# Optimization experiments

Measured on AMD Instinct MI355X. Metric: run time of the kernel, lower is better.

Reference implementation:

```python
import jax, jax.numpy as jnp
import numpy as np

EPS = 1e-5


def conv_bn_relu(x, W, b, g, be):
    # 3x3 SAME conv, NCHW / OIHW, followed by training-mode BatchNorm and ReLU
    y = jax.lax.conv_general_dilated(
        x, W, window_strides=(1, 1), padding='SAME',
        dimension_numbers=('NCHW', 'OIHW', 'NCHW'))
    y = y + b[None, :, None, None]
    m = y.mean(axis=(0, 2, 3), keepdims=True)
    v = y.var(axis=(0, 2, 3), keepdims=True)  # biased var, as torch BN uses
    y = (y - m) * jax.lax.rsqrt(v + EPS)
    y = y * g[None, :, None, None] + be[None, :, None, None]
    return jax.nn.relu(y)


def setup_inputs() -> dict:
    key = jax.random.key(0)
    ks = jax.random.split(key, 16)
    B, M, D = 512, 256, 100
    inp = {
        'F_channel': jax.random.normal(ks[0], (B, 2, 20, 20), jnp.float32),
        'G_real': jax.random.normal(ks[1], (B, M, D), jnp.float32),
        'G_imag': jax.random.normal(ks[2], (B, M, D), jnp.float32),
        'hr_real': jax.random.normal(ks[3], (B, D), jnp.float32),
        'hr_imag': jax.random.normal(ks[4], (B, D), jnp.float32),
    }
    chans = [(2, 128), (128, 64), (64, 64), (64, 32)]
    for i, (ci, co) in enumerate(chans):
        fan = ci * 9
        inp[f'W{i+1}'] = jax.random.normal(ks[5 + i], (co, ci, 3, 3), jnp.float32) / np.sqrt(fan)
        inp[f'b{i+1}'] = jnp.zeros((co,), jnp.float32)
        inp[f'g{i+1}'] = jnp.ones((co,), jnp.float32)
        inp[f'be{i+1}'] = jnp.zeros((co,), jnp.float32)
    inp['Wo'] = jax.random.normal(ks[9], (200, 12800), jnp.float32) / np.sqrt(12800)
    inp['bo'] = jnp.zeros((200,), jnp.float32)
    return inp


def reference(F_channel, G_real, G_imag, hr_real, hr_imag,
              W1, b1, g1, be1, W2, b2, g2, be2,
              W3, b3, g3, be3, W4, b4, g4, be4, Wo, bo):
    out = conv_bn_relu(F_channel, W1, b1, g1, be1)
    out = conv_bn_relu(out, W2, b2, g2, be2)
    out = conv_bn_relu(out, W3, b3, g3, be3)
    out = conv_bn_relu(out, W4, b4, g4, be4)
    out = out.reshape(out.shape[0], -1)          # [B, 12800], NCHW flatten matches torch view
    out = out @ Wo.T + bo                        # [B, 200]

    theta1, theta2 = out[:, :100], out[:, 100:]
    c = jnp.cos(theta1)                          # Re(Theta)  [B, D]
    s = jnp.sin(theta2)                          # Im(Theta)  [B, D]

    # diag_embed + matmul == elementwise scale of G columns by Theta (complex)
    Ar = G_real * c[:, None, :] - G_imag * s[:, None, :]   # [B, M, D]
    Ai = G_real * s[:, None, :] + G_imag * c[:, None, :]

    # matmul with hr (complex): t2 = sum_d A[b,m,d] * hr[b,d]
    t2r = jnp.einsum('bmd,bd->bm', Ar, hr_real) - jnp.einsum('bmd,bd->bm', Ai, hr_imag)
    t2i = jnp.einsum('bmd,bd->bm', Ar, hr_imag) + jnp.einsum('bmd,bd->bm', Ai, hr_real)

    B = out.shape[0]  # D_row = Theta.size(0) = batch
    norm_sq = jnp.sum(t2r * t2r + t2i * t2i)
    return -norm_sq / B
```

## Files before the change

kernel.cpp:

```cpp
#include <hip/hip_runtime.h>
#include <math.h>

typedef __bf16 bf16x8 __attribute__((ext_vector_type(8)));
typedef float f32x4 __attribute__((ext_vector_type(4)));
typedef unsigned short ushort8 __attribute__((ext_vector_type(8)));

__device__ __forceinline__ float bf2f(unsigned short u){ return __uint_as_float(((unsigned)u) << 16); }
__device__ __forceinline__ unsigned short f2bf(float f){
  unsigned v = __float_as_uint(f);
  return (unsigned short)((v + 0x7FFFu + ((v >> 16) & 1u)) >> 16);
}

__global__ void packw1_kernel(const float* __restrict__ W1, unsigned short* __restrict__ Wpk1)
{
  int idx = blockIdx.x*256 + threadIdx.x;
  if (idx >= 512) return;
  int lane = idx & 63, ct = idx >> 6;
  int co = ct*16 + (lane & 15);
  int lq = lane >> 4;
#pragma unroll
  for (int j = 0; j < 8; ++j){
    int k = lq*8 + j;
    Wpk1[(size_t)idx*8 + j] = (k < 18) ? f2bf(W1[(size_t)co*18 + k]) : (unsigned short)0;
  }
}

__global__ __launch_bounds__(256, 2) void conv1_mfma(
    const float* __restrict__ F, const unsigned short* __restrict__ Wpk1,
    const float* __restrict__ b1, unsigned short* __restrict__ y1,
    float* __restrict__ stats)
{
  __shared__ float xp[2*484];
  __shared__ float sred[256];
  const int tid = threadIdx.x, b = blockIdx.x;
  const int wid = tid >> 6, lane = tid & 63, lq = lane >> 4, lr = lane & 15;

  for (int i = tid; i < 256; i += 256) sred[i] = 0.f;
  for (int i = tid; i < 968; i += 256) xp[i] = 0.f;
  __syncthreads();
  for (int i = tid; i < 800; i += 256){
    int ci = i / 400, p = i - ci*400;
    xp[ci*484 + (p/20 + 1)*22 + (p%20) + 1] = F[((size_t)b*2 + ci)*400 + p];
  }
  __syncthreads();

  bf16x8 af[8];
#pragma unroll
  for (int ct = 0; ct < 8; ++ct)
    af[ct] = *(const bf16x8*)(Wpk1 + (size_t)(ct*64 + lane)*8);

  int off[8]; bool kval[8];
#pragma unroll
  for (int j = 0; j < 8; ++j){
    int k = lq*8 + j;
    kval[j] = (k < 18);
    int kc = kval[j] ? k : 0;
    int ci = kc / 9, dhw = kc - ci*9;
    off[j] = ci*484 + (dhw/3)*22 + (dhw - (dhw/3)*3);
  }

  f32x4 bias[8];
#pragma unroll
  for (int ct = 0; ct < 8; ++ct)
    bias[ct] = *(const f32x4*)(b1 + ct*16 + lq*4);

  float smv[8][4], sqv[8][4];
#pragma unroll
  for (int ct = 0; ct < 8; ++ct)
#pragma unroll
    for (int r = 0; r < 4; ++r){ smv[ct][r] = 0.f; sqv[ct][r] = 0.f; }

  for (int pt = wid; pt < 25; pt += 4){
    const int px = pt*16 + lr;
    const int h = px/20, w = px - (px/20)*20;
    const int base = h*22 + w;
    union { unsigned short u[8]; bf16x8 h8; } bfr;
#pragma unroll
    for (int j = 0; j < 8; ++j){
      float xv = kval[j] ? xp[base + off[j]] : 0.f;
      bfr.u[j] = f2bf(xv);
    }
    f32x4 zero4 = {0.f,0.f,0.f,0.f};
#pragma unroll
    for (int ct = 0; ct < 8; ++ct){
      f32x4 acc = __builtin_amdgcn_mfma_f32_16x16x32_bf16(af[ct], bfr.h8, zero4, 0, 0, 0);
      f32x4 y = acc + bias[ct];
      union { unsigned short u[4]; unsigned long long ll; } pk;
#pragma unroll
      for (int r = 0; r < 4; ++r){
        pk.u[r] = f2bf(y[r]);
        smv[ct][r] += y[r];
        sqv[ct][r] = fmaf(y[r], y[r], sqv[ct][r]);
      }
      *(unsigned long long*)(y1 + ((size_t)b*400 + px)*128 + ct*16 + lq*4) = pk.ll;
    }
  }

#pragma unroll
  for (int ct = 0; ct < 8; ++ct)
#pragma unroll
    for (int r = 0; r < 4; ++r){
      float v = smv[ct][r], q = sqv[ct][r];
#pragma unroll
      for (int m = 1; m < 16; m <<= 1){ v += __shfl_xor(v, m); q += __shfl_xor(q, m); }
      if (lr == 0){
        int co = ct*16 + lq*4 + r;
        atomicAdd(&sred[co], v);
        atomicAdd(&sred[128 + co], q);
      }
    }
  __syncthreads();
  float* st = stats + (size_t)(b & 3) * 256;
  for (int i = tid; i < 256; i += 256)
    atomicAdd(&st[i], sred[i]);
}

__global__ void bn_fin(const float* __restrict__ stats, const float* __restrict__ g,
                       const float* __restrict__ be, float* __restrict__ ss,
                       int C, float invN, int nsl)
{
  int c = threadIdx.x;
  if (c < C){
    float s = 0.f, q = 0.f;
    for (int t = 0; t < nsl; ++t){ s += stats[t*2*C + c]; q += stats[t*2*C + C + c]; }
    float mean = s * invN;
    float var  = q * invN - mean * mean;
    float sc   = g[c] * rsqrtf(var + 1e-5f);
    ss[c]      = sc;
    ss[C + c]  = be[c] - mean * sc;
  }
}

__global__ void packw_kernel(const float* __restrict__ W, unsigned short* __restrict__ Wpk,
                             int CT, int CIN, int total)
{
  int idx = blockIdx.x*256 + threadIdx.x;
  if (idx >= total) return;
  int lane = idx & 63;
  int t2 = idx >> 6;
  int dhw = t2 % 9;
  int t3 = t2 / 9;
  int ct = t3 % CT;
  int p  = t3 / CT;
  int co = ct*16 + (lane & 15);
  int ci0 = p*32 + (lane >> 4)*8;
#pragma unroll
  for (int j = 0; j < 8; ++j)
    Wpk[(size_t)idx*8 + j] = f2bf(W[((size_t)co*CIN + ci0 + j)*9 + dhw]);
}

template<int CIN, int COUT>
__global__ __launch_bounds__(512, 4) void conv_mfma(
    const unsigned short* __restrict__ xin, const float* __restrict__ ss_in,
    const unsigned short* __restrict__ Wpk, const float* __restrict__ bconv,
    unsigned short* __restrict__ yout, float* __restrict__ stats)
{
  constexpr int NCC = CIN/32;
  constexpr int CT  = COUT/16;
  constexpr int WCH = CT*9*64;
  __shared__ unsigned short xs[484*5*8];
  __shared__ unsigned short wl[WCH*8];
  __shared__ float sred[2*COUT];

  const int tid = threadIdx.x, b = blockIdx.x;
  const int wid = tid >> 6, lane = tid & 63, lq = lane >> 4, lr = lane & 15;

  for (int i = tid; i < 2*COUT; i += 512) sred[i] = 0.f;

  int pp[4];
#pragma unroll
  for (int s = 0; s < 4; ++s){
    int tile = (s < 3) ? (wid + 8*s) : 24;
    int px = tile*16 + lr;
    int prow = px/20, pcol = px - prow*20;
    pp[s] = (prow + 1)*22 + (pcol + 1);
  }

  f32x4 acc[CT][4];
#pragma unroll
  for (int ct = 0; ct < CT; ++ct)
#pragma unroll
    for (int s = 0; s < 4; ++s){ acc[ct][s][0]=0.f; acc[ct][s][1]=0.f; acc[ct][s][2]=0.f; acc[ct][s][3]=0.f; }

  const int oct = tid & 3;

  for (int p = 0; p < NCC; ++p){
    __syncthreads();
    for (int i = tid; i < WCH; i += 512)
      *(uint4*)&wl[(size_t)i*8] = *(const uint4*)(Wpk + ((size_t)p*WCH + i)*8);
    {
      const int c = p*32 + oct*8;
      f32x4 s0 = *(const f32x4*)(ss_in + c);
      f32x4 s1 = *(const f32x4*)(ss_in + c + 4);
      f32x4 h0 = *(const f32x4*)(ss_in + CIN + c);
      f32x4 h1 = *(const f32x4*)(ss_in + CIN + c + 4);
      for (int i = tid; i < 484*4; i += 512){
        int pidx = i >> 2;
        int r22 = pidx/22, c22 = pidx - r22*22;
        int row = r22 - 1, col = c22 - 1;
        union { unsigned short u[8]; uint4 v; } pk;
        if ((unsigned)row < 20u && (unsigned)col < 20u){
          ushort8 raw = *(const ushort8*)(xin + ((size_t)b*400 + row*20 + col)*CIN + c);
          pk.u[0] = f2bf(fmaxf(fmaf(bf2f(raw[0]), s0[0], h0[0]), 0.f));
          pk.u[1] = f2bf(fmaxf(fmaf(bf2f(raw[1]), s0[1], h0[1]), 0.f));
          pk.u[2] = f2bf(fmaxf(fmaf(bf2f(raw[2]), s0[2], h0[2]), 0.f));
          pk.u[3] = f2bf(fmaxf(fmaf(bf2f(raw[3]), s0[3], h0[3]), 0.f));
          pk.u[4] = f2bf(fmaxf(fmaf(bf2f(raw[4]), s1[0], h1[0]), 0.f));
          pk.u[5] = f2bf(fmaxf(fmaf(bf2f(raw[5]), s1[1], h1[1]), 0.f));
          pk.u[6] = f2bf(fmaxf(fmaf(bf2f(raw[6]), s1[2], h1[2]), 0.f));
          pk.u[7] = f2bf(fmaxf(fmaf(bf2f(raw[7]), s1[3], h1[3]), 0.f));
        } else {
          pk.v.x = 0u; pk.v.y = 0u; pk.v.z = 0u; pk.v.w = 0u;
        }
        *(uint4*)&xs[(size_t)(pidx*5 + oct)*8] = pk.v;
      }
    }
    __syncthreads();

#pragma unroll
    for (int dhw = 0; dhw < 9; ++dhw){
      const int doff = (dhw/3 - 1)*22 + (dhw - (dhw/3)*3 - 1);
      bf16x8 af[CT];
#pragma unroll
      for (int ct = 0; ct < CT; ++ct)
        af[ct] = *(const bf16x8*)&wl[(size_t)((ct*9 + dhw)*64 + lane)*8];
#pragma unroll
      for (int s = 0; s < 4; ++s){
        bf16x8 bf = *(const bf16x8*)&xs[(size_t)((pp[s] + doff)*5 + lq)*8];
#pragma unroll
        for (int ct = 0; ct < CT; ++ct)
          acc[ct][s] = __builtin_amdgcn_mfma_f32_16x16x32_bf16(af[ct], bf, acc[ct][s], 0, 0, 0);
      }
    }
  }

  float smv[CT][4], sqv[CT][4];
#pragma unroll
  for (int ct = 0; ct < CT; ++ct)
#pragma unroll
    for (int r = 0; r < 4; ++r){ smv[ct][r] = 0.f; sqv[ct][r] = 0.f; }

#pragma unroll
  for (int ct = 0; ct < CT; ++ct){
    f32x4 bias = *(const f32x4*)(bconv + ct*16 + lq*4);
#pragma unroll
    for (int s = 0; s < 4; ++s){
      const bool valid = (s < 3) || (wid == 0);
      const int tile = (s < 3) ? (wid + 8*s) : 24;
      const int px = tile*16 + lr;
      f32x4 y = acc[ct][s] + bias;
      union { unsigned short u[4]; unsigned long long ll; } pk;
#pragma unroll
      for (int r = 0; r < 4; ++r){
        float yv = valid ? y[r] : 0.f;
        pk.u[r] = f2bf(y[r]);
        smv[ct][r] += yv;
        sqv[ct][r] = fmaf(yv, yv, sqv[ct][r]);
      }
      if (valid)
        *(unsigned long long*)(yout + ((size_t)b*400 + px)*COUT + ct*16 + lq*4) = pk.ll;
    }
  }
#pragma unroll
  for (int ct = 0; ct < CT; ++ct)
#pragma unroll
    for (int r = 0; r < 4; ++r){
      float v = smv[ct][r], w2 = sqv[ct][r];
#pragma unroll
      for (int m = 1; m < 16; m <<= 1){ v += __shfl_xor(v, m); w2 += __shfl_xor(w2, m); }
      if (lr == 0){
        int co = ct*16 + lq*4 + r;
        atomicAdd(&sred[co], v);
        atomicAdd(&sred[COUT + co], w2);
      }
    }
  __syncthreads();
  float* st = stats + (size_t)(b & 3) * 2 * COUT;
  for (int i = tid; i < 2*COUT; i += 512)
    atomicAdd(&st[i], sred[i]);
}

__global__ __launch_bounds__(256) void wopack_kernel(const float* __restrict__ Wo,
                                                     unsigned short* __restrict__ Wob)
{
  __shared__ float row[12800];
  const int j = blockIdx.x, tid = threadIdx.x;
  if (j < 200){
    const float4* src = (const float4*)(Wo + (size_t)j*12800);
    for (int i = tid; i < 3200; i += 256) ((float4*)row)[i] = src[i];
    __syncthreads();
    for (int ko = tid; ko < 1600; ko += 256){
      int p = ko >> 2, c0 = (ko & 3)*8;
      union { unsigned short u[8]; uint4 v; } pk;
#pragma unroll
      for (int t = 0; t < 8; ++t) pk.u[t] = f2bf(row[(c0+t)*400 + p]);
      *(uint4*)(Wob + (size_t)j*12800 + ko*8) = pk.v;
    }
  } else {
    uint4 z = {0,0,0,0};
    for (int ko = tid; ko < 1600; ko += 256)
      *(uint4*)(Wob + (size_t)j*12800 + ko*8) = z;
  }
}

__global__ __launch_bounds__(256, 4) void linear_mfma(
    const unsigned short* __restrict__ y4, const float* __restrict__ ss4,
    const unsigned short* __restrict__ Wob, float* __restrict__ lin_z)
{
  __shared__ unsigned short As[64*128];
  __shared__ unsigned short Bs[64*128];
  const int tid = threadIdx.x;
  const int m0 = blockIdx.x * 64;
  const int j0 = blockIdx.y * 64;
  const int z  = blockIdx.z;
  const int wid = tid >> 6, lane = tid & 63, lq = lane >> 4, lr = lane & 15;
  const int srow = tid >> 4, soct = tid & 15;
  const int c0 = (soct & 3) * 8;

  f32x4 s0 = *(const f32x4*)(ss4 + c0);
  f32x4 s1 = *(const f32x4*)(ss4 + c0 + 4);
  f32x4 h0 = *(const f32x4*)(ss4 + 32 + c0);
  f32x4 h1 = *(const f32x4*)(ss4 + 32 + c0 + 4);

  f32x4 acc[4];
#pragma unroll
  for (int ct = 0; ct < 4; ++ct){ acc[ct][0]=0.f; acc[ct][1]=0.f; acc[ct][2]=0.f; acc[ct][3]=0.f; }

  for (int ch = 0; ch < 4; ++ch){
    const int k0 = z*512 + ch*128;
    __syncthreads();
#pragma unroll
    for (int pass = 0; pass < 4; ++pass){
      int row = pass*16 + srow;
      ushort8 raw = *(const ushort8*)(y4 + (size_t)(m0+row)*12800 + k0 + soct*8);
      union { unsigned short u[8]; uint4 v; } pk;
      pk.u[0] = f2bf(fmaxf(fmaf(bf2f(raw[0]), s0[0], h0[0]), 0.f));
      pk.u[1] = f2bf(fmaxf(fmaf(bf2f(raw[1]), s0[1], h0[1]), 0.f));
      pk.u[2] = f2bf(fmaxf(fmaf(bf2f(raw[2]), s0[2], h0[2]), 0.f));
      pk.u[3] = f2bf(fmaxf(fmaf(bf2f(raw[3]), s0[3], h0[3]), 0.f));
      pk.u[4] = f2bf(fmaxf(fmaf(bf2f(raw[4]), s1[0], h1[0]), 0.f));
      pk.u[5] = f2bf(fmaxf(fmaf(bf2f(raw[5]), s1[1], h1[1]), 0.f));
      pk.u[6] = f2bf(fmaxf(fmaf(bf2f(raw[6]), s1[2], h1[2]), 0.f));
      pk.u[7] = f2bf(fmaxf(fmaf(bf2f(raw[7]), s1[3], h1[3]), 0.f));
      *(uint4*)&As[(size_t)((row << 4) + (soct ^ (row & 7)))*8] = pk.v;
      uint4 wv = *(const uint4*)(Wob + (size_t)(j0+row)*12800 + k0 + soct*8);
      *(uint4*)&Bs[(size_t)((row << 4) + (soct ^ (row & 7)))*8] = wv;
    }
    __syncthreads();
#pragma unroll
    for (int ks = 0; ks < 4; ++ks){
      const int arow = wid*16 + lr;
      bf16x8 afr = *(const bf16x8*)&As[(size_t)((arow << 4) + ((ks*4 + lq) ^ (arow & 7)))*8];
#pragma unroll
      for (int ct = 0; ct < 4; ++ct){
        const int brow = ct*16 + lr;
        bf16x8 bfr = *(const bf16x8*)&Bs[(size_t)((brow << 4) + ((ks*4 + lq) ^ (brow & 7)))*8];
        acc[ct] = __builtin_amdgcn_mfma_f32_16x16x32_bf16(afr, bfr, acc[ct], 0, 0, 0);
      }
    }
  }
#pragma unroll
  for (int ct = 0; ct < 4; ++ct){
    int j = j0 + ct*16 + lr;
    if (j < 208){
#pragma unroll
      for (int r = 0; r < 4; ++r){
        int m = m0 + wid*16 + lq*4 + r;
        lin_z[((size_t)z*512 + m)*208 + j] = acc[ct][r];
      }
    }
  }
}

__global__ __launch_bounds__(1024, 2) void phase_kernel(const float* __restrict__ lin_z,
                                                        const float* __restrict__ bo,
                                                        const float* __restrict__ Gr,
                                                        const float* __restrict__ Gi,
                                                        const float* __restrict__ hrr,
                                                        const float* __restrict__ hri,
                                                        float* __restrict__ accum)
{
  const int b = blockIdx.x;
  const int tid = threadIdx.x;
  __shared__ float psum[4][200];
  __shared__ float lsh[200];
  __shared__ float u[100];
  __shared__ float pq[100];
  __shared__ float wred[16];

  if (tid < 800){
    int zq = tid / 200, j = tid - zq*200;
    int z0 = (zq == 0) ? 0 : (6*zq + 1);
    int zn = (zq == 0) ? 7 : 6;
    float a = 0.f;
    for (int z = z0; z < z0 + zn; ++z)
      a += lin_z[((size_t)z*512 + b)*208 + j];
    psum[zq][j] = a;
  }
  __syncthreads();
  if (tid < 200)
    lsh[tid] = bo[tid] + psum[0][tid] + psum[1][tid] + psum[2][tid] + psum[3][tid];
  __syncthreads();
  if (tid < 100){
    float c = cosf(lsh[tid]);
    float s = sinf(lsh[100 + tid]);
    float hr = hrr[b*100 + tid];
    float hi = hri[b*100 + tid];
    u[tid]  = c*hr - s*hi;
    pq[tid] = c*hi + s*hr;
  }
  __syncthreads();

  const int m = tid >> 2, q = tid & 3;
  const float4* grow  = (const float4*)(Gr + ((size_t)b*256 + m)*100);
  const float4* girow = (const float4*)(Gi + ((size_t)b*256 + m)*100);
  float tr = 0.f, ti = 0.f;
#pragma unroll
  for (int k = 0; k < 6; ++k){
    int i = q + 4*k;
    float4 g  = grow[i];
    float4 gg = girow[i];
    float4 uu = *(const float4*)&u[i*4];
    float4 qq = *(const float4*)&pq[i*4];
    tr += g.x*uu.x - gg.x*qq.x;  ti += g.x*qq.x + gg.x*uu.x;
    tr += g.y*uu.y - gg.y*qq.y;  ti += g.y*qq.y + gg.y*uu.y;
    tr += g.z*uu.z - gg.z*qq.z;  ti += g.z*qq.z + gg.z*uu.z;
    tr += g.w*uu.w - gg.w*qq.w;  ti += g.w*qq.w + gg.w*uu.w;
  }
  if (q == 0){
    float4 g  = grow[24];
    float4 gg = girow[24];
    float4 uu = *(const float4*)&u[96];
    float4 qq = *(const float4*)&pq[96];
    tr += g.x*uu.x - gg.x*qq.x;  ti += g.x*qq.x + gg.x*uu.x;
    tr += g.y*uu.y - gg.y*qq.y;  ti += g.y*qq.y + gg.y*uu.y;
    tr += g.z*uu.z - gg.z*qq.z;  ti += g.z*qq.z + gg.z*uu.z;
    tr += g.w*uu.w - gg.w*qq.w;  ti += g.w*qq.w + gg.w*uu.w;
  }
  tr += __shfl_xor(tr, 1); tr += __shfl_xor(tr, 2);
  ti += __shfl_xor(ti, 1); ti += __shfl_xor(ti, 2);
  float ns = (q == 0) ? (tr*tr + ti*ti) : 0.f;
#pragma unroll
  for (int off = 4; off < 64; off <<= 1) ns += __shfl_down(ns, off);
  if ((tid & 63) == 0) wred[tid >> 6] = ns;
  __syncthreads();
  if (tid == 0){
    float t = 0.f;
#pragma unroll
    for (int w = 0; w < 16; ++w) t += wred[w];
    atomicAdd(accum, t);
  }
}

__global__ void finalize_kernel(const float* __restrict__ accum, float* __restrict__ out)
{
  out[0] = -accum[0] * (1.0f / 512.0f);
}

extern "C" void kernel_launch(void* const* d_in, const int* in_sizes, int n_in,
                              void* d_out, int out_size, void* d_ws, size_t ws_size,
                              hipStream_t stream)
{
  const float* F   = (const float*)d_in[0];
  const float* Gr  = (const float*)d_in[1];
  const float* Gi  = (const float*)d_in[2];
  const float* hrr = (const float*)d_in[3];
  const float* hri = (const float*)d_in[4];
  const float* W1  = (const float*)d_in[5];
  const float* b1  = (const float*)d_in[6];
  const float* g1  = (const float*)d_in[7];
  const float* be1 = (const float*)d_in[8];
  const float* W2  = (const float*)d_in[9];
  const float* b2  = (const float*)d_in[10];
  const float* g2  = (const float*)d_in[11];
  const float* be2 = (const float*)d_in[12];
  const float* W3  = (const float*)d_in[13];
  const float* b3  = (const float*)d_in[14];
  const float* g3  = (const float*)d_in[15];
  const float* be3 = (const float*)d_in[16];
  const float* W4  = (const float*)d_in[17];
  const float* b4  = (const float*)d_in[18];
  const float* g4  = (const float*)d_in[19];
  const float* be4 = (const float*)d_in[20];
  const float* Wo  = (const float*)d_in[21];
  const float* bo  = (const float*)d_in[22];

  char* ws = (char*)d_ws;
  unsigned short* y1   = (unsigned short*)(ws);
  unsigned short* y2   = (unsigned short*)(ws + 52428800);
  unsigned short* y3   = (unsigned short*)(ws);
  unsigned short* y4   = (unsigned short*)(ws + 52428800);
  unsigned short* Wob  = (unsigned short*)(ws + 65536000);
  float*          lin_z= (float*)(ws + 13107200);
  float* stats = (float*)(ws + 78643200);
  float* ssb   = (float*)(ws + 78652416);
  float* accum = (float*)(ws + 78656512);
  unsigned short* Wpk1 = (unsigned short*)(ws + 78656528);
  unsigned short* Wpk2 = (unsigned short*)(ws + 78664720);
  unsigned short* Wpk3 = (unsigned short*)(ws + 78812176);
  unsigned short* Wpk4 = (unsigned short*)(ws + 78885904);

  hipMemsetAsync(ws + 78643200, 0, 13328, stream);

  const float invN = 1.0f / 204800.0f;

  packw1_kernel<<<2, 256, 0, stream>>>(W1, Wpk1);
  packw_kernel<<<36, 256, 0, stream>>>(W2, Wpk2, 4, 128, 9216);
  packw_kernel<<<18, 256, 0, stream>>>(W3, Wpk3, 4, 64, 4608);
  packw_kernel<<< 9, 256, 0, stream>>>(W4, Wpk4, 2, 64, 2304);

  conv1_mfma<<<512, 256, 0, stream>>>(F, Wpk1, b1, y1, stats);
  bn_fin<<<1, 128, 0, stream>>>(stats, g1, be1, ssb, 128, invN, 4);

  conv_mfma<128, 64><<<512, 512, 0, stream>>>(y1, ssb, Wpk2, b2, y2, stats + 1024);
  bn_fin<<<1, 64, 0, stream>>>(stats + 1024, g2, be2, ssb + 256, 64, invN, 4);

  conv_mfma<64, 64><<<512, 512, 0, stream>>>(y2, ssb + 256, Wpk3, b3, y3, stats + 1536);
  bn_fin<<<1, 64, 0, stream>>>(stats + 1536, g3, be3, ssb + 384, 64, invN, 4);

  conv_mfma<64, 32><<<512, 512, 0, stream>>>(y3, ssb + 384, Wpk4, b4, y4, stats + 2048);
  bn_fin<<<1, 32, 0, stream>>>(stats + 2048, g4, be4, ssb + 512, 32, invN, 4);

  wopack_kernel<<<256, 256, 0, stream>>>(Wo, Wob);

  linear_mfma<<<dim3(8, 4, 25), 256, 0, stream>>>(y4, ssb + 512, Wob, lin_z);

  phase_kernel<<<512, 1024, 0, stream>>>(lin_z, bo, Gr, Gi, hrr, hri, accum);
  finalize_kernel<<<1, 1, 0, stream>>>(accum, (float*)d_out);
}
```

Measured before the change: 204.2 us.

## Prefetch next channel chunk into registers during MFMA compute in conv kernel

Restructures the per-chunk loop of the MFMA conv kernel so the global loads of the next 32-channel input chunk go into registers before the current chunk's MFMA compute. The BN-ReLU transform and LDS write then happen after compute. This hides global memory latency behind the matrix math. It also skips the redundant fourth tile's MFMAs for waves other than wave 0. The cost is extra register pressure from the prefetch buffers, which could hurt occupancy under launch_bounds(512,4).

```diff
diff --git a/kernel.cpp b/kernel.cpp
--- a/kernel.cpp
+++ b/kernel.cpp
@@ -164,6 +164,7 @@
 
   const int tid = threadIdx.x, b = blockIdx.x;
   const int wid = tid >> 6, lane = tid & 63, lq = lane >> 4, lr = lane & 15;
+  const int oct = tid & 3;
 
   for (int i = tid; i < 2*COUT; i += 512) sred[i] = 0.f;
 
@@ -182,41 +183,59 @@
 #pragma unroll
     for (int s = 0; s < 4; ++s){ acc[ct][s][0]=0.f; acc[ct][s][1]=0.f; acc[ct][s][2]=0.f; acc[ct][s][3]=0.f; }
 
-  const int oct = tid & 3;
-
-  for (int p = 0; p < NCC; ++p){
-    __syncthreads();
-    for (int i = tid; i < WCH; i += 512)
-      *(uint4*)&wl[(size_t)i*8] = *(const uint4*)(Wpk + ((size_t)p*WCH + i)*8);
-    {
-      const int c = p*32 + oct*8;
-      f32x4 s0 = *(const f32x4*)(ss_in + c);
-      f32x4 s1 = *(const f32x4*)(ss_in + c + 4);
-      f32x4 h0 = *(const f32x4*)(ss_in + CIN + c);
-      f32x4 h1 = *(const f32x4*)(ss_in + CIN + c + 4);
-      for (int i = tid; i < 484*4; i += 512){
+  auto LOADA = [&](int p, uint4 (&ar)[4]){
+#pragma unroll
+    for (int k = 0; k < 4; ++k){
+      int i = tid + k*512;
+      if (i < 1936){
+        int pidx = i >> 2;
+        int r22 = pidx/22, c22 = pidx - r22*22;
+        int row = r22 - 1, col = c22 - 1;
+        if ((unsigned)row < 20u && (unsigned)col < 20u)
+          ar[k] = *(const uint4*)(xin + ((size_t)b*400 + row*20 + col)*CIN + p*32 + oct*8);
+      }
+    }
+  };
+  auto WRITEA = [&](int p, uint4 (&ar)[4]){
+    const int c = p*32 + oct*8;
+    f32x4 s0 = *(const f32x4*)(ss_in + c);
+    f32x4 s1 = *(const f32x4*)(ss_in + c + 4);
+    f32x4 h0 = *(const f32x4*)(ss_in + CIN + c);
+    f32x4 h1 = *(const f32x4*)(ss_in + CIN + c + 4);
+#pragma unroll
+    for (int k = 0; k < 4; ++k){
+      int i = tid + k*512;
+      if (i < 1936){
         int pidx = i >> 2;
         int r22 = pidx/22, c22 = pidx - r22*22;
         int row = r22 - 1, col = c22 - 1;
         union { unsigned short u[8]; uint4 v; } pk;
         if ((unsigned)row < 20u && (unsigned)col < 20u){
-          ushort8 raw = *(const ushort8*)(xin + ((size_t)b*400 + row*20 + col)*CIN + c);
-          pk.u[0] = f2bf(fmaxf(fmaf(bf2f(raw[0]), s0[0], h0[0]), 0.f));
-          pk.u[1] = f2bf(fmaxf(fmaf(bf2f(raw[1]), s0[1], h0[1]), 0.f));
-          pk.u[2] = f2bf(fmaxf(fmaf(bf2f(raw[2]), s0[2], h0[2]), 0.f));
-          pk.u[3] = f2bf(fmaxf(fmaf(bf2f(raw[3]), s0[3], h0[3]), 0.f));
-          pk.u[4] = f2bf(fmaxf(fmaf(bf2f(raw[4]), s1[0], h1[0]), 0.f));
-          pk.u[5] = f2bf(fmaxf(fmaf(bf2f(raw[5]), s1[1], h1[1]), 0.f));
-          pk.u[6] = f2bf(fmaxf(fmaf(bf2f(raw[6]), s1[2], h1[2]), 0.f));
-          pk.u[7] = f2bf(fmaxf(fmaf(bf2f(raw[7]), s1[3], h1[3]), 0.f));
+          union { uint4 v; ushort8 h; } rw; rw.v = ar[k];
+          pk.u[0] = f2bf(fmaxf(fmaf(bf2f(rw.h[0]), s0[0], h0[0]), 0.f));
+          pk.u[1] = f2bf(fmaxf(fmaf(bf2f(rw.h[1]), s0[1], h0[1]), 0.f));
+          pk.u[2] = f2bf(fmaxf(fmaf(bf2f(rw.h[2]), s0[2], h0[2]), 0.f));
+          pk.u[3] = f2bf(fmaxf(fmaf(bf2f(rw.h[3]), s0[3], h0[3]), 0.f));
+          pk.u[4] = f2bf(fmaxf(fmaf(bf2f(rw.h[4]), s1[0], h1[0]), 0.f));
+          pk.u[5] = f2bf(fmaxf(fmaf(bf2f(rw.h[5]), s1[1], h1[1]), 0.f));
+          pk.u[6] = f2bf(fmaxf(fmaf(bf2f(rw.h[6]), s1[2], h1[2]), 0.f));
+          pk.u[7] = f2bf(fmaxf(fmaf(bf2f(rw.h[7]), s1[3], h1[3]), 0.f));
         } else {
           pk.v.x = 0u; pk.v.y = 0u; pk.v.z = 0u; pk.v.w = 0u;
         }
         *(uint4*)&xs[(size_t)(pidx*5 + oct)*8] = pk.v;
       }
     }
-    __syncthreads();
-
+  };
+  auto STAGEW = [&](int p){
+#pragma unroll
+    for (int k = 0; k < 5; ++k){
+      int i = tid + k*512;
+      if (i < WCH)
+        *(uint4*)&wl[(size_t)i*8] = *(const uint4*)(Wpk + ((size_t)p*WCH + i)*8);
+    }
+  };
+  auto COMPUTE = [&](){
 #pragma unroll
     for (int dhw = 0; dhw < 9; ++dhw){
       const int doff = (dhw/3 - 1)*22 + (dhw - (dhw/3)*3 - 1);
@@ -226,11 +245,32 @@
         af[ct] = *(const bf16x8*)&wl[(size_t)((ct*9 + dhw)*64 + lane)*8];
 #pragma unroll
       for (int s = 0; s < 4; ++s){
+        if (s == 3 && wid != 0) continue;
         bf16x8 bf = *(const bf16x8*)&xs[(size_t)((pp[s] + doff)*5 + lq)*8];
 #pragma unroll
         for (int ct = 0; ct < CT; ++ct)
           acc[ct][s] = __builtin_amdgcn_mfma_f32_16x16x32_bf16(af[ct], bf, acc[ct][s], 0, 0, 0);
       }
+    }
+  };
+
+  {
+    uint4 arA[4];
+    LOADA(0, arA);
+    STAGEW(0);
+    WRITEA(0, arA);
+  }
+  __syncthreads();
+
+  for (int p = 0; p < NCC; ++p){
+    uint4 arB[4];
+    if (p + 1 < NCC) LOADA(p + 1, arB);
+    COMPUTE();
+    __syncthreads();
+    if (p + 1 < NCC){
+      STAGEW(p + 1);
+      WRITEA(p + 1, arB);
+      __syncthreads();
     }
   }
 
```

Measured after the change: 256.7 us. 25.7% more time.
